# Kernel tuning notes

Hardware: AMD Instinct MI355X
Metric: run time of the kernel (lower is better)

Reference implementation:

```python
import jax, jax.numpy as jnp
import numpy as np

HEADS, HEAD_DIM, DIM = 8, 64, 512
KSIZES = [3, 5, 7]
GROUPS = [2, 3, 3]  # heads per kernel size


def _dwconv(x, w, b, k):
    # x: (b, C, H, W), w: (C, 1, k, k) depthwise, b: (C,)
    p = k // 2
    y = jax.lax.conv_general_dilated(
        x, w, window_strides=(1, 1), padding=((p, p), (p, p)),
        dimension_numbers=("NCHW", "OIHW", "NCHW"),
        feature_group_count=x.shape[1])
    return y + b[None, :, None, None]


def setup_inputs() -> dict:
    key = jax.random.key(0)
    ks = jax.random.split(key, 8)
    b, H, W = 32, 32, 32
    n = H * W + 1
    return {
        "x": jax.random.normal(ks[0], (b, n, DIM), jnp.float32),
        "W_qkv": jax.random.normal(ks[1], (DIM, 3 * DIM), jnp.float32) * 0.02,
        "b_qkv": jnp.zeros((3 * DIM,), jnp.float32),
        "conv_w3": jax.random.normal(ks[2], (GROUPS[0] * HEAD_DIM, 1, 3, 3), jnp.float32) * 0.1,
        "conv_b3": jnp.zeros((GROUPS[0] * HEAD_DIM,), jnp.float32),
        "conv_w5": jax.random.normal(ks[3], (GROUPS[1] * HEAD_DIM, 1, 5, 5), jnp.float32) * 0.1,
        "conv_b5": jnp.zeros((GROUPS[1] * HEAD_DIM,), jnp.float32),
        "conv_w7": jax.random.normal(ks[4], (GROUPS[2] * HEAD_DIM, 1, 7, 7), jnp.float32) * 0.1,
        "conv_b7": jnp.zeros((GROUPS[2] * HEAD_DIM,), jnp.float32),
        "W_out": jax.random.normal(ks[5], (DIM, DIM), jnp.float32) * 0.02,
        "b_out": jnp.zeros((DIM,), jnp.float32),
        "H": 32,
        "W": 32,
    }


def reference(x, W_qkv, b_qkv, conv_w3, conv_b3, conv_w5, conv_b5,
              conv_w7, conv_b7, W_out, b_out, H, W):
    b, n, dim = x.shape
    qkv = x @ W_qkv + b_qkv                         # (b, n, 3*dim)
    q, k, v = jnp.split(qkv, 3, axis=-1)

    def to_heads(t):
        return t.reshape(b, n, HEADS, HEAD_DIM).transpose(0, 2, 1, 3)  # (b,h,n,d)

    q, k, v = to_heads(q), to_heads(k), to_heads(v)

    # Factorized (linear) attention: softmax over tokens on K, then K^T V context
    k_sm = jax.nn.softmax(k, axis=2)                 # softmax over n
    context = jnp.einsum("bhnp,bhnq->bhpq", k_sm, v)  # (b,h,d,d)
    factor = jnp.einsum("bhnp,bhpq->bhnq", q * (HEAD_DIM ** -0.5), context)

    # Convolutional relative position encoding on V (drop CLS token)
    v_img = v[:, :, 1:, :]                            # (b,h,HW,d)
    v_img = v_img.transpose(0, 1, 3, 2).reshape(b, HEADS * HEAD_DIM, H, W)
    split_pts = np.cumsum([g * HEAD_DIM for g in GROUPS])[:-1].tolist()
    parts = jnp.split(v_img, split_pts, axis=1)
    convs = [(conv_w3, conv_b3), (conv_w5, conv_b5), (conv_w7, conv_b7)]
    outs = [_dwconv(p, w, bb, kk) for p, (w, bb), kk in zip(parts, convs, KSIZES)]
    ev = jnp.concatenate(outs, axis=1)                # (b, h*d, H, W)
    ev = ev.reshape(b, HEADS, HEAD_DIM, H * W).transpose(0, 1, 3, 2)  # (b,h,HW,d)
    ev = jnp.concatenate(
        [jnp.zeros((b, HEADS, 1, HEAD_DIM), ev.dtype), ev], axis=2)   # re-add CLS
    crpe = q * ev                                     # elementwise (CoaT CRPE)

    out = (factor + crpe).transpose(0, 2, 1, 3).reshape(b, n, dim)
    return out @ W_out + b_out
```

## Files before the change

### kernel.cpp

```cpp
#include <hip/hip_runtime.h>
#include <stdint.h>
#include <stddef.h>

#define DEV __device__ __forceinline__

using bf16x8 = __attribute__((ext_vector_type(8))) __bf16;
using f32x4  = __attribute__((ext_vector_type(4))) float;
typedef unsigned short u16;
typedef unsigned int   u32;
using u16x8 = __attribute__((ext_vector_type(8))) unsigned short;

constexpr int CB    = 32;
constexpr int CN    = 1025;
constexpr int CD    = 512;
constexpr int CH    = 8;
constexpr int CHD   = 64;
constexpr int MROWS = CB*CN;
constexpr int MPAD  = 32896;
constexpr int NQKV  = 1536;
constexpr int NCH   = 5;
constexpr float L2E = 1.4426950408889634f;

DEV float bf2f(u16 u){ union{u32 i; float f;} x; x.i = ((u32)u)<<16; return x.f; }
DEV u16 f2bf(float f){ union{float f; u32 i;} x; x.f = f; u32 r = x.i + 0x7fffu + ((x.i>>16)&1u); return (u16)(r>>16); }

DEV f32x4 mfma16(bf16x8 a, bf16x8 b, f32x4 c){
  return __builtin_amdgcn_mfma_f32_16x16x32_bf16(a, b, c, 0, 0, 0);
}

typedef const __attribute__((address_space(1))) u32 GA;
typedef __attribute__((address_space(3))) u32 LA;
DEV void gload_lds16(const void* g, void* l){
  __builtin_amdgcn_global_load_lds((GA*)g, (LA*)l, 16, 0, 0);
}

__global__ void cast_pad_x(const float* __restrict__ x, u16* __restrict__ xb){
  size_t stride = (size_t)gridDim.x * blockDim.x;
  size_t tot4  = (size_t)MPAD * CD / 4;
  size_t real4 = (size_t)MROWS * CD / 4;
  for(size_t i4 = (size_t)blockIdx.x*blockDim.x + threadIdx.x; i4 < tot4; i4 += stride){
    ushort4 o;
    if(i4 < real4){
      float4 f = reinterpret_cast<const float4*>(x)[i4];
      o.x=f2bf(f.x); o.y=f2bf(f.y); o.z=f2bf(f.z); o.w=f2bf(f.w);
    } else { o.x=0; o.y=0; o.z=0; o.w=0; }
    reinterpret_cast<ushort4*>(xb)[i4] = o;
  }
}

template<int R, int C>
__global__ void transpose_cast(const float* __restrict__ in, u16* __restrict__ out){
  __shared__ float t[32][33];
  int bx = blockIdx.x % (C/32);
  int by = blockIdx.x / (C/32);
  int c0 = bx*32, r0 = by*32;
  int j = threadIdx.x & 31, i0 = threadIdx.x >> 5;
  for(int i=i0;i<32;i+=8) t[i][j] = in[(size_t)(r0+i)*C + c0 + j];
  __syncthreads();
  for(int i=i0;i<32;i+=8) out[(size_t)(c0+i)*R + r0 + j] = f2bf(t[j][i]);
}

template<int NCOL, int MODE>
__global__ __launch_bounds__(256)
void gemm_k(const u16* __restrict__ A, const u16* __restrict__ BT,
            const float* __restrict__ bias,
            u16* __restrict__ qo, u16* __restrict__ ko, u16* __restrict__ vo,
            float* __restrict__ outf)
{
  constexpr int K  = CD;
  constexpr int NT = NCOL/128;
  int nwg = gridDim.x, bid = blockIdx.x;
  int qg = nwg >> 3, rr = nwg & 7;
  int xc = bid & 7, ii = bid >> 3;
  int lt = (xc < rr ? xc*(qg+1) : rr*(qg+1) + (xc-rr)*qg) + ii;
  int mt = lt / NT, nt = lt - mt*NT;
  int m0 = mt*128, n0 = nt*128;

  __shared__ u16 lds[2*128*32];
  u16* As = lds;
  u16* Bs = lds + 128*32;
  int tid = threadIdx.x, wave = tid>>6, lane = tid&63;
  int l15 = lane&15, kg = lane>>4;
  int wm = wave&1, wn = wave>>1;
  int srow = lane>>2, sslot = lane&3;

  f32x4 acc[4][4];
  #pragma unroll
  for(int a0=0;a0<4;a0++)
    #pragma unroll
    for(int b0=0;b0<4;b0++) acc[a0][b0] = f32x4{0.f,0.f,0.f,0.f};

  for(int k0=0;k0<K;k0+=32){
    #pragma unroll
    for(int it=0;it<2;it++){
      int chunk = wave*2 + it;
      int row = chunk*16 + srow;
      int sl = sslot ^ ((row>>1)&3);
      gload_lds16(A  + (size_t)(m0+row)*K + k0 + sl*8, As + chunk*512);
      gload_lds16(BT + (size_t)(n0+row)*K + k0 + sl*8, Bs + chunk*512);
    }
    __syncthreads();
    bf16x8 af[4], bfr[4];
    #pragma unroll
    for(int mi=0;mi<4;mi++){
      int row = wm*64 + mi*16 + l15;
      int sl = kg ^ ((row>>1)&3);
      af[mi] = *reinterpret_cast<const bf16x8*>((const char*)As + row*64 + sl*16);
    }
    #pragma unroll
    for(int ni=0;ni<4;ni++){
      int row = wn*64 + ni*16 + l15;
      int sl = kg ^ ((row>>1)&3);
      bfr[ni] = *reinterpret_cast<const bf16x8*>((const char*)Bs + row*64 + sl*16);
    }
    #pragma unroll
    for(int mi=0;mi<4;mi++)
      #pragma unroll
      for(int ni=0;ni<4;ni++)
        acc[mi][ni] = mfma16(af[mi], bfr[ni], acc[mi][ni]);
    __syncthreads();
  }

  #pragma unroll
  for(int mi=0;mi<4;mi++){
    #pragma unroll
    for(int i=0;i<4;i++){
      int r = m0 + wm*64 + mi*16 + kg*4 + i;
      if(r >= MROWS) continue;
      int bb = r / CN;
      int nn = r - bb*CN;
      #pragma unroll
      for(int ni=0;ni<4;ni++){
        int c = n0 + wn*64 + ni*16 + l15;
        float val = acc[mi][ni][i] + bias[c];
        if constexpr (MODE==0){
          int which = c >> 9;
          int h = (c>>6)&7, d = c&63;
          if(which==1) val = exp2f(val*L2E);
          u16* dst = which==0 ? qo : (which==1 ? ko : vo);
          dst[(((size_t)bb*CH + h)*CN + nn)*CHD + d] = f2bf(val);
        } else {
          outf[(size_t)r*CD + c] = val;
        }
      }
    }
  }
}

__global__ void zero_ev(u16* __restrict__ ev){
  int i = blockIdx.x*256 + threadIdx.x;
  if(i < CB*CH*CHD){
    int bh = i >> 6, d = i & 63;
    ev[(size_t)bh*CN*CHD + d] = 0;
  }
}

__global__ __launch_bounds__(256)
void ctx_k(const u16* __restrict__ ekb, const u16* __restrict__ vb,
           float* __restrict__ Cpart, float* __restrict__ Spart)
{
  int blk = blockIdx.x;
  int bh = blk / NCH, t = blk - bh*NCH;
  const u16* ekbase = ekb + (size_t)bh*CN*CHD;
  const u16* vbase  = vb  + (size_t)bh*CN*CHD;
  __shared__ u16 ekT[64*128];
  __shared__ u16 vT [64*128];
  int tid = threadIdx.x, wave = tid>>6, lane = tid&63;
  int l15 = lane&15, kg = lane>>4;

  bf16x8 ones;
  #pragma unroll
  for(int j=0;j<8;j++) ones[j] = (__bf16)1.0f;

  f32x4 acc[4], accS[4];
  #pragma unroll
  for(int i=0;i<4;i++){ acc[i]=f32x4{0.f,0.f,0.f,0.f}; accS[i]=f32x4{0.f,0.f,0.f,0.f}; }

  for(int s=0;s<2;s++){
    int n0 = t*256 + s*128;
    __syncthreads();
    #pragma unroll
    for(int i=0;i<8;i++){
      int nl = lane*2 + (i&1);
      int p0 = wave*16 + (i>>1)*4;
      int n  = n0 + nl;
      ushort4 kv{0,0,0,0}, vv{0,0,0,0};
      if(n < CN){
        kv = *reinterpret_cast<const ushort4*>(ekbase + (size_t)n*CHD + p0);
        vv = *reinterpret_cast<const ushort4*>(vbase  + (size_t)n*CHD + p0);
      }
      u16 ks[4] = {kv.x,kv.y,kv.z,kv.w};
      u16 vs[4] = {vv.x,vv.y,vv.z,vv.w};
      #pragma unroll
      for(int j=0;j<4;j++){
        int p = p0 + j;
        int slot = (nl>>3) ^ (p&15);
        *(u16*)((char*)ekT + p*256 + slot*16 + (nl&7)*2) = ks[j];
        *(u16*)((char*)vT  + p*256 + slot*16 + (nl&7)*2) = vs[j];
      }
    }
    __syncthreads();
    #pragma unroll
    for(int kk2=0;kk2<4;kk2++){
      int bq = wave*16 + l15;
      bf16x8 bfr = *reinterpret_cast<const bf16x8*>((const char*)vT + bq*256 + (((kk2*4+kg)^(bq&15))*16));
      #pragma unroll
      for(int mi=0;mi<4;mi++){
        int p = mi*16 + l15;
        bf16x8 af = *reinterpret_cast<const bf16x8*>((const char*)ekT + p*256 + (((kk2*4+kg)^(p&15))*16));
        acc[mi]  = mfma16(af, bfr,  acc[mi]);
        accS[mi] = mfma16(af, ones, accS[mi]);
      }
    }
  }
  float* Cdst = Cpart + (size_t)blk*4096;
  #pragma unroll
  for(int mi=0;mi<4;mi++)
    #pragma unroll
    for(int i=0;i<4;i++){
      int pp = mi*16 + kg*4 + i;
      int qq = wave*16 + l15;
      Cdst[pp*64 + qq] = acc[mi][i];
      if(l15==0) Spart[(size_t)blk*64 + pp] = accS[mi][i];
    }
}

__global__ __launch_bounds__(256)
void combine_k(const float* __restrict__ Cpart, const float* __restrict__ Spart,
               u16* __restrict__ Ctb)
{
  int bh = blockIdx.x;
  __shared__ float Cs[4096];
  __shared__ float rcpS[64];
  int tid = threadIdx.x;
  for(int e=tid; e<4096; e+=256){
    float s = 0.f;
    #pragma unroll
    for(int t=0;t<NCH;t++) s += Cpart[((size_t)bh*NCH+t)*4096 + e];
    Cs[e] = s;
  }
  if(tid < 64){
    float s = 0.f;
    #pragma unroll
    for(int t=0;t<NCH;t++) s += Spart[((size_t)bh*NCH+t)*64 + tid];
    rcpS[tid] = 0.125f / s;
  }
  __syncthreads();
  #pragma unroll
  for(int it2=0; it2<2; it2++){
    int qq = it2*32 + (tid>>3);
    int sg = tid & 7;
    int pb = (sg ^ (qq&7))*8;
    u16x8 pack;
    #pragma unroll
    for(int j=0;j<8;j++) pack[j] = f2bf(Cs[(pb+j)*64 + qq] * rcpS[pb+j]);
    *reinterpret_cast<u16x8*>(Ctb + (size_t)bh*4096 + qq*64 + sg*8) = pack;
  }
}

template<int KS, int H0, int NHG, int BAND>
__global__ __launch_bounds__(512)
void conv_k(const u16* __restrict__ vb, const float* __restrict__ w,
            const float* __restrict__ bias, u16* __restrict__ ev)
{
  constexpr int R  = KS/2;
  constexpr int IW = 32 + 2*R;
  constexpr int IH = BAND + 2*R;
  constexpr int NB = 32/BAND;
  __shared__ u16 in_s[IH*IW*64];
  int band = blockIdx.x % NB;
  int bhi  = blockIdx.x / NB;
  int b = bhi / NHG;
  int hh = bhi - b*NHG;
  int h = H0 + hh;
  int y0 = band*BAND;
  const u16* src = vb + (((size_t)b*CH + h)*CN + 1)*CHD;
  int tid = threadIdx.x;
  int d = tid & 63;

  for(int e = tid; e < IH*IW*64; e += 512){
    int dd = e & 63;
    int rest = e >> 6;
    int xp = rest % IW;
    int yp = rest / IW;
    int gy = y0 + yp - R, gx = xp - R;
    u16 val = 0;
    if((unsigned)gy < 32u && (unsigned)gx < 32u) val = src[(size_t)(gy*32+gx)*CHD + dd];
    in_s[e] = val;
  }
  int c_local = hh*64 + d;
  float wreg[KS*KS];
  const float* wp = w + (size_t)c_local*KS*KS;
  #pragma unroll
  for(int i=0;i<KS*KS;i++) wreg[i] = wp[i];
  float bi = bias[c_local];
  __syncthreads();

  constexpr int GPR = 8/BAND;
  constexpr int XC  = 32/GPR;
  int grp = tid >> 6;
  int yl  = grp / GPR;
  int xs  = (grp - yl*GPR) * XC;
  u16* dst = ev + ((((size_t)b*CH + h)*CN) + 1 + (size_t)(y0+yl)*32)*CHD + d;
  for(int xi=0; xi<XC; xi++){
    int x = xs + xi;
    float acc = bi;
    #pragma unroll
    for(int ky=0;ky<KS;ky++)
      #pragma unroll
      for(int kx=0;kx<KS;kx++)
        acc = fmaf(wreg[ky*KS+kx], bf2f(in_s[((yl+ky)*IW + (x+kx))*64 + d]), acc);
    dst[(size_t)x*CHD] = f2bf(acc);
  }
}

__global__ __launch_bounds__(256)
void fuse_k(const u16* __restrict__ qb, const u16* __restrict__ Ctb,
            const u16* __restrict__ evb, u16* __restrict__ Aout)
{
  int blk = blockIdx.x;
  int bh = blk / 9, t = blk - bh*9;
  int b = bh >> 3, h = bh & 7;
  int n0 = t*128;
  __shared__ u16 Ct[64*64];
  __shared__ u16 qs[128*64];
  __shared__ u16 evs[128*64];
  int tid = threadIdx.x, wave = tid>>6, lane = tid&63;
  int l15 = lane&15, kg = lane>>4;

  #pragma unroll
  for(int it=0; it<2; it++){
    int cc = wave*2 + it;
    gload_lds16(Ctb + (size_t)bh*4096 + cc*512 + lane*8, (char*)Ct + cc*1024);
  }
  const u16* qbase  = qb  + (size_t)bh*CN*CHD;
  const u16* evbase = evb + (size_t)bh*CN*CHD;
  #pragma unroll
  for(int it=0; it<4; it++){
    int cc = wave*4 + it;
    int row = cc*8 + (lane>>3);
    int P = lane&7;
    int sl = P ^ (row&7);
    gload_lds16(qbase  + (size_t)(n0+row)*CHD + sl*8, (char*)qs  + cc*1024);
    gload_lds16(evbase + (size_t)(n0+row)*CHD + sl*8, (char*)evs + cc*1024);
  }
  __syncthreads();

  f32x4 acc[2][4];
  #pragma unroll
  for(int mi=0;mi<2;mi++)
    #pragma unroll
    for(int ni=0;ni<4;ni++) acc[mi][ni] = f32x4{0.f,0.f,0.f,0.f};

  #pragma unroll
  for(int kk2=0;kk2<2;kk2++){
    bf16x8 af[2];
    #pragma unroll
    for(int mi=0;mi<2;mi++){
      int rl = wave*32 + mi*16 + l15;
      int asl = (kk2*4+kg) ^ (rl&7);
      af[mi] = *reinterpret_cast<const bf16x8*>((const char*)qs + rl*128 + asl*16);
    }
    #pragma unroll
    for(int ni=0;ni<4;ni++){
      int brow = ni*16 + l15;
      int bsl = (kk2*4+kg) ^ (brow&7);
      bf16x8 bfr = *reinterpret_cast<const bf16x8*>((const char*)Ct + brow*128 + bsl*16);
      #pragma unroll
      for(int mi=0;mi<2;mi++)
        acc[mi][ni] = mfma16(af[mi], bfr, acc[mi][ni]);
    }
  }

  #pragma unroll
  for(int mi=0;mi<2;mi++){
    #pragma unroll
    for(int i=0;i<4;i++){
      int rl = wave*32 + mi*16 + kg*4 + i;
      int n = n0 + rl;
      if(n >= CN) continue;
      #pragma unroll
      for(int ni=0;ni<4;ni++){
        int dd = ni*16 + l15;
        int sl2 = (dd>>3) ^ (rl&7);
        float qv  = bf2f(*(const u16*)((const char*)qs  + rl*128 + sl2*16 + (dd&7)*2));
        float evv = bf2f(*(const u16*)((const char*)evs + rl*128 + sl2*16 + (dd&7)*2));
        Aout[((size_t)b*CN + n)*CD + h*64 + dd] = f2bf(acc[mi][ni][i] + qv*evv);
      }
    }
  }
}

extern "C" void kernel_launch(void* const* d_in, const int* in_sizes, int n_in,
                              void* d_out, int out_size, void* d_ws, size_t ws_size,
                              hipStream_t stream)
{
  const float* x    = (const float*)d_in[0];
  const float* Wqkv = (const float*)d_in[1];
  const float* bqkv = (const float*)d_in[2];
  const float* w3   = (const float*)d_in[3];
  const float* b3   = (const float*)d_in[4];
  const float* w5   = (const float*)d_in[5];
  const float* b5   = (const float*)d_in[6];
  const float* w7   = (const float*)d_in[7];
  const float* b7   = (const float*)d_in[8];
  const float* Wout = (const float*)d_in[9];
  const float* bout = (const float*)d_in[10];
  float* out = (float*)d_out;

  char* ws = (char*)d_ws;
  size_t off = 0;
  auto alloc = [&](size_t bytes)->void*{
    void* p = ws + off;
    off += (bytes + 255) & ~(size_t)255;
    return p;
  };
  u16* x_bf  = (u16*)alloc((size_t)MPAD*CD*2);
  u16* WqkvT = (u16*)alloc((size_t)NQKV*CD*2);
  u16* WoutT = (u16*)alloc((size_t)CD*CD*2);
  u16* q_bf  = (u16*)alloc((size_t)CB*CH*CN*CHD*2);
  u16* ek_bf = (u16*)alloc((size_t)CB*CH*CN*CHD*2);
  u16* v_bf  = (u16*)alloc((size_t)CB*CH*CN*CHD*2);
  u16* ev_bf = (u16*)alloc((size_t)CB*CH*CN*CHD*2);
  float* Cpart = (float*)alloc((size_t)CB*CH*NCH*4096*4);
  float* Spart = (float*)alloc((size_t)CB*CH*NCH*64*4);
  u16* Ctb   = (u16*)alloc((size_t)CB*CH*4096*2);
  u16* A_bf  = x_bf;

  cast_pad_x<<<2048, 256, 0, stream>>>(x, x_bf);
  transpose_cast<CD, NQKV><<<(CD/32)*(NQKV/32), 256, 0, stream>>>(Wqkv, WqkvT);
  transpose_cast<CD, CD><<<(CD/32)*(CD/32), 256, 0, stream>>>(Wout, WoutT);
  gemm_k<NQKV, 0><<<(MPAD/128)*(NQKV/128), 256, 0, stream>>>(x_bf, WqkvT, bqkv, q_bf, ek_bf, v_bf, nullptr);
  zero_ev<<<64, 256, 0, stream>>>(ev_bf);
  ctx_k<<<CB*CH*NCH, 256, 0, stream>>>(ek_bf, v_bf, Cpart, Spart);
  combine_k<<<CB*CH, 256, 0, stream>>>(Cpart, Spart, Ctb);
  conv_k<3, 0, 2, 8><<<CB*2*4, 512, 0, stream>>>(v_bf, w3, b3, ev_bf);
  conv_k<5, 2, 3, 8><<<CB*3*4, 512, 0, stream>>>(v_bf, w5, b5, ev_bf);
  conv_k<7, 5, 3, 4><<<CB*3*8, 512, 0, stream>>>(v_bf, w7, b7, ev_bf);
  fuse_k<<<CB*CH*9, 256, 0, stream>>>(q_bf, Ctb, ev_bf, A_bf);
  gemm_k<CD, 1><<<(MPAD/128)*(CD/128), 256, 0, stream>>>(A_bf, WoutT, bout, nullptr, nullptr, nullptr, out);

  (void)in_sizes; (void)n_in; (void)out_size; (void)ws_size;
}
```

Baseline: 447.7 us.

## Double-buffer GEMM LDS tiles and vectorize context and conv staging loads

The GEMM main loop now uses two LDS buffers, issuing global-to-LDS loads for the next K-step while MFMAs run on the current one, with one waitcnt+barrier per step instead of two syncthreads. The context kernel packs two token values into 32-bit LDS stores rather than 16-bit ones, and the conv kernel stages its input tile with 8-byte vector loads and stores instead of scalar u16 accesses. These target load latency exposure and LDS/global instruction count, at the cost of doubled GEMM LDS usage, which may reduce occupancy.

```diff
diff --git a/kernel.cpp b/kernel.cpp
--- a/kernel.cpp
+++ b/kernel.cpp
@@ -68,6 +68,7 @@
             float* __restrict__ outf)
 {
   constexpr int K  = CD;
+  constexpr int KSTEPS = K/32;
   constexpr int NT = NCOL/128;
   int nwg = gridDim.x, bid = blockIdx.x;
   int qg = nwg >> 3, rr = nwg & 7;
@@ -76,9 +77,7 @@
   int mt = lt / NT, nt = lt - mt*NT;
   int m0 = mt*128, n0 = nt*128;
 
-  __shared__ u16 lds[2*128*32];
-  u16* As = lds;
-  u16* Bs = lds + 128*32;
+  __shared__ u16 lds[4*4096];
   int tid = threadIdx.x, wave = tid>>6, lane = tid&63;
   int l15 = lane&15, kg = lane>>4;
   int wm = wave&1, wn = wave>>1;
@@ -90,7 +89,9 @@
     #pragma unroll
     for(int b0=0;b0<4;b0++) acc[a0][b0] = f32x4{0.f,0.f,0.f,0.f};
 
-  for(int k0=0;k0<K;k0+=32){
+  auto stage = [&](int buf, int k0){
+    u16* As = lds + buf*8192;
+    u16* Bs = As + 4096;
     #pragma unroll
     for(int it=0;it<2;it++){
       int chunk = wave*2 + it;
@@ -99,7 +100,10 @@
       gload_lds16(A  + (size_t)(m0+row)*K + k0 + sl*8, As + chunk*512);
       gload_lds16(BT + (size_t)(n0+row)*K + k0 + sl*8, Bs + chunk*512);
     }
-    __syncthreads();
+  };
+  auto compute = [&](int buf){
+    const u16* As = lds + buf*8192;
+    const u16* Bs = As + 4096;
     bf16x8 af[4], bfr[4];
     #pragma unroll
     for(int mi=0;mi<4;mi++){
@@ -118,8 +122,18 @@
       #pragma unroll
       for(int ni=0;ni<4;ni++)
         acc[mi][ni] = mfma16(af[mi], bfr[ni], acc[mi][ni]);
-    __syncthreads();
-  }
+  };
+
+  stage(0, 0);
+  asm volatile("s_waitcnt vmcnt(0)\n\ts_barrier" ::: "memory");
+  int cur = 0;
+  for(int t=0; t<KSTEPS-1; ++t){
+    stage(cur^1, (t+1)*32);
+    compute(cur);
+    asm volatile("s_waitcnt vmcnt(0)\n\ts_barrier" ::: "memory");
+    cur ^= 1;
+  }
+  compute(cur);
 
   #pragma unroll
   for(int mi=0;mi<4;mi++){
@@ -179,24 +193,31 @@
   for(int s=0;s<2;s++){
     int n0 = t*256 + s*128;
     __syncthreads();
-    #pragma unroll
-    for(int i=0;i<8;i++){
-      int nl = lane*2 + (i&1);
-      int p0 = wave*16 + (i>>1)*4;
-      int n  = n0 + nl;
-      ushort4 kv{0,0,0,0}, vv{0,0,0,0};
+    int n  = n0 + lane*2;
+    int hi = (lane*2)>>3;
+    int off = ((lane*2)&7)*2;
+    #pragma unroll
+    for(int i2=0;i2<4;i2++){
+      int p0 = wave*16 + i2*4;
+      ushort4 k0{0,0,0,0}, k1{0,0,0,0}, v0{0,0,0,0}, v1{0,0,0,0};
       if(n < CN){
-        kv = *reinterpret_cast<const ushort4*>(ekbase + (size_t)n*CHD + p0);
-        vv = *reinterpret_cast<const ushort4*>(vbase  + (size_t)n*CHD + p0);
-      }
-      u16 ks[4] = {kv.x,kv.y,kv.z,kv.w};
-      u16 vs[4] = {vv.x,vv.y,vv.z,vv.w};
+        k0 = *reinterpret_cast<const ushort4*>(ekbase + (size_t)n*CHD + p0);
+        v0 = *reinterpret_cast<const ushort4*>(vbase  + (size_t)n*CHD + p0);
+      }
+      if(n+1 < CN){
+        k1 = *reinterpret_cast<const ushort4*>(ekbase + (size_t)(n+1)*CHD + p0);
+        v1 = *reinterpret_cast<const ushort4*>(vbase  + (size_t)(n+1)*CHD + p0);
+      }
+      u16 ks0[4]={k0.x,k0.y,k0.z,k0.w}, ks1[4]={k1.x,k1.y,k1.z,k1.w};
+      u16 vs0[4]={v0.x,v0.y,v0.z,v0.w}, vs1[4]={v1.x,v1.y,v1.z,v1.w};
       #pragma unroll
       for(int j=0;j<4;j++){
         int p = p0 + j;
-        int slot = (nl>>3) ^ (p&15);
-        *(u16*)((char*)ekT + p*256 + slot*16 + (nl&7)*2) = ks[j];
-        *(u16*)((char*)vT  + p*256 + slot*16 + (nl&7)*2) = vs[j];
+        int slot = hi ^ (p&15);
+        u32 kw = (u32)ks0[j] | ((u32)ks1[j]<<16);
+        u32 vw = (u32)vs0[j] | ((u32)vs1[j]<<16);
+        *(u32*)((char*)ekT + p*256 + slot*16 + off) = kw;
+        *(u32*)((char*)vT  + p*256 + slot*16 + off) = vw;
       }
     }
     __syncthreads();
@@ -278,15 +299,16 @@
   int tid = threadIdx.x;
   int d = tid & 63;
 
-  for(int e = tid; e < IH*IW*64; e += 512){
-    int dd = e & 63;
-    int rest = e >> 6;
+  for(int e4 = tid; e4 < IH*IW*16; e4 += 512){
+    int dd4 = e4 & 15;
+    int rest = e4 >> 4;
     int xp = rest % IW;
     int yp = rest / IW;
     int gy = y0 + yp - R, gx = xp - R;
-    u16 val = 0;
-    if((unsigned)gy < 32u && (unsigned)gx < 32u) val = src[(size_t)(gy*32+gx)*CHD + dd];
-    in_s[e] = val;
+    ushort4 val{0,0,0,0};
+    if((unsigned)gy < 32u && (unsigned)gx < 32u)
+      val = *reinterpret_cast<const ushort4*>(src + (size_t)(gy*32+gx)*CHD + dd4*4);
+    *reinterpret_cast<ushort4*>(in_s + (yp*IW+xp)*64 + dd4*4) = val;
   }
   int c_local = hh*64 + d;
   float wreg[KS*KS];
```

After: 387.4 us. -13.5%, faster.
